# Optimization experiments

Measured on AMD Instinct MI355X. Metric: run time of the kernel, lower is better.

## Reference

```python
import jax, jax.numpy as jnp
import numpy as np

B, F, H, OUT, S = 32768, 256, 128, 64, 6
RELAX, EPS, BN_EPS = 1.5, 1e-05, 1e-05
SQRT_HALF = 0.7071067811865476


def _bn(h, g, b):
    # training-mode BatchNorm1d: biased batch statistics over dim 0
    m = h.mean(axis=0)
    v = h.var(axis=0)
    return (h - m) * jax.lax.rsqrt(v + BN_EPS) * g + b


def _tfrm(x, W, g, b, glu_act=True):
    h = _bn(x @ W, g, b)
    if glu_act:
        d = h.shape[1] // 2
        h = h[:, :d] * jax.nn.sigmoid(h[:, d:])
    return h


def setup_inputs() -> dict:
    key = jax.random.key(0)
    ks = jax.random.split(key, 6)
    f32 = jnp.float32
    return {
        "x": jax.random.normal(ks[0], (B, F), f32),
        "enc_g": jnp.ones((F,), f32), "enc_b": jnp.zeros((F,), f32),
        "W1": jax.random.normal(ks[1], (F, 2 * H), f32) * 0.05,
        "g1": jnp.ones((2 * H,), f32), "b1": jnp.zeros((2 * H,), f32),
        "W2": jax.random.normal(ks[2], (H, 2 * H), f32) * 0.05,
        "g2": jnp.ones((2 * H,), f32), "b2": jnp.zeros((2 * H,), f32),
        "W3": jax.random.normal(ks[3], (S, H, 2 * H), f32) * 0.05,
        "g3": jnp.ones((S, 2 * H), f32), "b3": jnp.zeros((S, 2 * H), f32),
        "W4": jax.random.normal(ks[4], (S, H, 2 * H), f32) * 0.05,
        "g4": jnp.ones((S, 2 * H), f32), "b4": jnp.zeros((S, 2 * H), f32),
        "Wc": jax.random.normal(ks[5], (S - 1, OUT, F), f32) * 0.05,
        "gc": jnp.ones((S - 1, F), f32), "bc": jnp.zeros((S - 1, F), f32),
    }


def reference(x, enc_g, enc_b, W1, g1, b1, W2, g2, b2, W3, g3, b3,
              W4, g4, b4, Wc, gc, bc):
    x = _bn(x, enc_g, enc_b)                      # [B, F]
    masked = x
    compl = jnp.ones((x.shape[0], F), x.dtype)    # complementary aggregated mask
    agg_out, agg_entropy = [], []
    for ni in range(S):
        h = _tfrm(masked, W1, g1, b1)                             # [B, H]
        h = (_tfrm(h, W2, g2, b2) + h) * SQRT_HALF
        h = (_tfrm(h, W3[ni], g3[ni], b3[ni]) + h) * SQRT_HALF
        h = (_tfrm(h, W4[ni], g4[ni], b4[ni]) + h) * SQRT_HALF
        if ni > 0:
            # NOTE: source uses x (not h) here -- replicated faithfully
            agg_out.append(jax.nn.relu(x[:, :OUT]))
        fc = h[:, OUT:]                                           # [B, OUT]
        if ni < S - 1:
            coef = _tfrm(fc, Wc[ni], gc[ni], bc[ni], glu_act=False)  # [B, F]
            mask_values = jax.nn.softmax(coef * compl, axis=1)
            compl = compl * (RELAX - mask_values)
            agg_entropy.append(
                jnp.mean(jnp.sum(-mask_values * jnp.log(mask_values + EPS), axis=1))
                / (S - 1))
            masked = mask_values * x
    out = jnp.sum(jnp.stack(agg_out, axis=0), axis=0)   # [B, OUT]
    entropy = jnp.sum(jnp.stack(agg_entropy))           # scalar
    return (out, entropy)
```

## Files before the change

kernel.cpp:

```cpp
#include <hip/hip_runtime.h>
#include <math.h>

#define BSZ   32768
#define FDIM  256
#define HDIM  128
#define OUTD  64
#define SQRT_HALF 0.70710678118654752f
#define BN_EPS 1e-5f
#define SM_EPS 1e-5f
#define INV_B (1.0f / 32768.0f)
#define NCPY  8
#define SLOT  (NCPY * 512)

typedef __attribute__((ext_vector_type(8))) short bf16x8;
typedef __attribute__((ext_vector_type(4))) short bf16x4;
typedef __attribute__((ext_vector_type(4))) float f32x4;

__device__ __forceinline__ float b2f(unsigned short u) {
    return __uint_as_float(((unsigned int)u) << 16);
}
__device__ __forceinline__ unsigned short f2b(float f) {
    unsigned int u = __float_as_uint(f);
    u += 0x7fff + ((u >> 16) & 1);
    return (unsigned short)(u >> 16);
}

__device__ __forceinline__ void async16(const void* g, void* l) {
    __builtin_amdgcn_global_load_lds(
        (const __attribute__((address_space(1))) void*)(uintptr_t)g,
        (__attribute__((address_space(3))) void*)(unsigned int)(uintptr_t)l,
        16, 0, 0);
}

__device__ inline float waveMaxAll(float v) {
#pragma unroll
    for (int m = 32; m > 0; m >>= 1) v = fmaxf(v, __shfl_xor(v, m, 64));
    return v;
}
__device__ inline float waveSumAll(float v) {
#pragma unroll
    for (int m = 32; m > 0; m >>= 1) v += __shfl_xor(v, m, 64);
    return v;
}

__global__ __launch_bounds__(256) void prep_w(
    const float* __restrict__ W1, const float* __restrict__ W2,
    const float* __restrict__ W3, const float* __restrict__ W4,
    const float* __restrict__ Wc,
    unsigned short* __restrict__ W1t, unsigned short* __restrict__ W2t,
    unsigned short* __restrict__ W3t, unsigned short* __restrict__ W4t,
    unsigned short* __restrict__ Wct)
{
    const int m = blockIdx.x, kz = blockIdx.y, n = threadIdx.x;
    const float* src; unsigned short* dst; int K;
    if (m == 0)      { src = W1;                        dst = W1t;               K = 256; }
    else if (m == 1) { src = W2;                        dst = W2t;               K = 128; }
    else if (m < 7)  { int i = m - 2;  src = W3 + (size_t)i * 128 * 256; dst = W3t + (size_t)i * 32768; K = 128; }
    else if (m < 12) { int i = m - 7;  src = W4 + (size_t)i * 128 * 256; dst = W4t + (size_t)i * 32768; K = 128; }
    else             { int i = m - 12; src = Wc + (size_t)i * 64 * 256;  dst = Wct + (size_t)i * 16384; K = 64; }
    const int k0 = kz * 32;
    if (k0 >= K) return;
    for (int k = k0; k < k0 + 32; ++k)
        dst[(size_t)n * K + k] = f2b(src[(size_t)k * 256 + n]);
}

__global__ __launch_bounds__(256) void colstats(const float* __restrict__ X,
                                                float* __restrict__ st0) {
    __shared__ float red[4][512];
    const int sub = threadIdx.x >> 6;
    const int c4  = (threadIdx.x & 63) << 2;
    float s[4] = {0.f, 0.f, 0.f, 0.f}, q[4] = {0.f, 0.f, 0.f, 0.f};
#pragma unroll 8
    for (int i = 0; i < 8; ++i) {
        const int row = blockIdx.x * 32 + i * 4 + sub;
        float4 v = *(const float4*)(X + (size_t)row * 256 + c4);
        s[0] += v.x; q[0] += v.x * v.x;
        s[1] += v.y; q[1] += v.y * v.y;
        s[2] += v.z; q[2] += v.z * v.z;
        s[3] += v.w; q[3] += v.w * v.w;
    }
#pragma unroll
    for (int e = 0; e < 4; ++e) {
        red[sub][c4 + e] = s[e];
        red[sub][256 + c4 + e] = q[e];
    }
    __syncthreads();
    const int t = threadIdx.x;
    const int cp = (blockIdx.x & (NCPY - 1)) * 512;
    float sS = red[0][t] + red[1][t] + red[2][t] + red[3][t];
    float sQ = red[0][256 + t] + red[1][256 + t] + red[2][256 + t] + red[3][256 + t];
    atomicAdd(&st0[cp + t], sS);
    atomicAdd(&st0[cp + 256 + t], sQ);
}

__global__ __launch_bounds__(256) void norm_x(const float* __restrict__ x,
                                              const float* __restrict__ st0,
                                              const float* __restrict__ g,
                                              const float* __restrict__ b,
                                              unsigned short* __restrict__ xb,
                                              float* __restrict__ out) {
    const int i4 = blockIdx.x * 256 + threadIdx.x;
    const int row = i4 >> 6, c4 = (i4 & 63) << 2;
    float4 xv = *(const float4*)(x + (size_t)row * 256 + c4);
    float sS[4] = {0.f, 0.f, 0.f, 0.f}, sQ[4] = {0.f, 0.f, 0.f, 0.f};
#pragma unroll
    for (int cp = 0; cp < NCPY; ++cp) {
        float4 a = *(const float4*)&st0[cp * 512 + c4];
        float4 q = *(const float4*)&st0[cp * 512 + 256 + c4];
        sS[0] += a.x; sS[1] += a.y; sS[2] += a.z; sS[3] += a.w;
        sQ[0] += q.x; sQ[1] += q.y; sQ[2] += q.z; sQ[3] += q.w;
    }
    float4 gv = *(const float4*)&g[c4];
    float4 bv = *(const float4*)&b[c4];
    const float* xp = (const float*)&xv;
    const float* gp = (const float*)&gv; const float* bp = (const float*)&bv;
    float n[4];
    ushort4 ob;
    unsigned short* obp = (unsigned short*)&ob;
#pragma unroll
    for (int e = 0; e < 4; ++e) {
        float mean = sS[e] * INV_B;
        float var  = sQ[e] * INV_B - mean * mean;
        float sc   = gp[e] * rsqrtf(var + BN_EPS);
        float sh   = bp[e] - mean * sc;
        n[e] = xp[e] * sc + sh;
        obp[e] = f2b(n[e]);
    }
    *(ushort4*)(xb + (size_t)row * 256 + c4) = ob;
    if (c4 < OUTD) {
        float4 ov = make_float4(5.0f * fmaxf(n[0], 0.f), 5.0f * fmaxf(n[1], 0.f),
                                5.0f * fmaxf(n[2], 0.f), 5.0f * fmaxf(n[3], 0.f));
        *(float4*)(out + (size_t)row * OUTD + c4) = ov;
    }
}

__device__ __forceinline__ void gemm_epilogue(
    f32x4 (&acc)[2][4], int row0, int wave, int lane, int tid, int bcp,
    float* redS, float* redQ,
    unsigned short* __restrict__ Pout, float* __restrict__ statsOut)
{
    const int fm = lane & 15;
    const int orow = row0 + (lane >> 4) * 4;
    const int ocol = wave * 64 + fm;
#pragma unroll
    for (int i = 0; i < 2; ++i)
#pragma unroll
        for (int j = 0; j < 4; ++j)
#pragma unroll
            for (int r = 0; r < 4; ++r)
                Pout[(size_t)(orow + i * 16 + r) * 256 + (ocol + j * 16)] = f2b(acc[i][j][r]);

#pragma unroll
    for (int j = 0; j < 4; ++j) {
        float s = 0.f, q = 0.f;
#pragma unroll
        for (int i = 0; i < 2; ++i)
#pragma unroll
            for (int r = 0; r < 4; ++r) {
                float v = acc[i][j][r];
                s += v; q += v * v;
            }
        s += __shfl_xor(s, 16, 64); s += __shfl_xor(s, 32, 64);
        q += __shfl_xor(q, 16, 64); q += __shfl_xor(q, 32, 64);
        if (lane < 16) {
            redS[wave * 64 + j * 16 + lane] = s;
            redQ[wave * 64 + j * 16 + lane] = q;
        }
    }
    __syncthreads();
    atomicAdd(&statsOut[bcp + tid], redS[tid]);
    atomicAdd(&statsOut[bcp + 256 + tid], redQ[tid]);
}

__global__ __launch_bounds__(256) void gemm_bf16(
    const unsigned short* __restrict__ A,
    const unsigned short* __restrict__ Wt, int K,
    unsigned short* __restrict__ P,
    float* __restrict__ statsOut)
{
    __shared__ short As[32 * 32];
    __shared__ short Bs[256 * 32];
    __shared__ float redS[256], redQ[256];

    const int tid  = threadIdx.x;
    const int wave = tid >> 6;
    const int lane = tid & 63;
    const int row0 = blockIdx.x * 32;
    const int bcp  = (blockIdx.x & (NCPY - 1)) * 512;

    const int sr = lane >> 2;
    const int sc = (lane & 3) * 8;
    const int fm = lane & 15;
    const int fq = (lane >> 4) * 8;

    f32x4 acc[2][4];
#pragma unroll
    for (int i = 0; i < 2; ++i)
#pragma unroll
        for (int j = 0; j < 4; ++j)
            acc[i][j] = (f32x4){0.f, 0.f, 0.f, 0.f};

    for (int k0 = 0; k0 < K; k0 += 32) {
        if (wave < 2)
            async16(A + (size_t)(row0 + wave * 16 + sr) * K + k0 + sc,
                    (void*)(As + wave * 512 + lane * 8));
#pragma unroll
        for (int t = 0; t < 4; ++t) {
            const int wr = wave * 64 + t * 16 + sr;
            async16(Wt + (size_t)wr * K + k0 + sc,
                    (void*)(Bs + (wave * 4 + t) * 512 + lane * 8));
        }
        __syncthreads();

        bf16x8 af[2], bfr[4];
#pragma unroll
        for (int i = 0; i < 2; ++i)
            af[i] = *(const bf16x8*)(As + (i * 16 + fm) * 32 + fq);
#pragma unroll
        for (int j = 0; j < 4; ++j)
            bfr[j] = *(const bf16x8*)(Bs + (wave * 64 + j * 16 + fm) * 32 + fq);
#pragma unroll
        for (int i = 0; i < 2; ++i)
#pragma unroll
            for (int j = 0; j < 4; ++j)
                acc[i][j] = __builtin_amdgcn_mfma_f32_16x16x32_bf16(af[i], bfr[j], acc[i][j], 0, 0, 0);
        __syncthreads();
    }

    gemm_epilogue(acc, row0, wave, lane, tid, bcp, redS, redQ, P, statsOut);
}

template <int MODE>
__global__ __launch_bounds__(256) void gemm_mask(
    const unsigned short* Pc,
    const float* __restrict__ cstats,
    const float* __restrict__ gc, const float* __restrict__ bc,
    const unsigned short* __restrict__ xb,
    unsigned short* __restrict__ cmpl,
    float* __restrict__ ent,
    const unsigned short* __restrict__ Wt,
    unsigned short* Pout,
    float* __restrict__ statsOut)
{
    __shared__ short Am[32 * 256];
    __shared__ short Bs[256 * 32];
    __shared__ float redS[256], redQ[256];
    __shared__ float tScl[256], tShf[256];
    __shared__ float went[4];

    const int tid  = threadIdx.x;
    const int wave = tid >> 6;
    const int lane = tid & 63;
    const int row0 = blockIdx.x * 32;
    const int bcp  = (blockIdx.x & (NCPY - 1)) * 512;

    const int sr = lane >> 2;
    const int sc = (lane & 3) * 8;

#pragma unroll
    for (int t = 0; t < 4; ++t) {
        const int wr = wave * 64 + t * 16 + sr;
        async16(Wt + (size_t)wr * 256 + sc,
                (void*)(Bs + (wave * 4 + t) * 512 + lane * 8));
    }

    {
        float s = 0.f, q = 0.f;
#pragma unroll
        for (int cp = 0; cp < NCPY; ++cp) {
            s += cstats[cp * 512 + tid];
            q += cstats[cp * 512 + 256 + tid];
        }
        float mean = s * INV_B, var = q * INV_B - mean * mean;
        float scl_ = gc[tid] * rsqrtf(var + BN_EPS);
        tScl[tid] = scl_;
        tShf[tid] = bc[tid] - mean * scl_;
    }
    __syncthreads();

    const int r  = tid >> 3;
    const int cq = tid & 7;
    const size_t grow = (size_t)(row0 + r) * 256;

    float l[32];
    float mx = -1e30f;
#pragma unroll
    for (int e = 0; e < 4; ++e) {
        const int c = cq * 32 + e * 8;
        bf16x8 pv = *(const bf16x8*)(Pc + grow + c);
        bf16x8 cv;
        if (MODE) cv = *(const bf16x8*)(cmpl + grow + c);
        float4 s0 = *(const float4*)&tScl[c], s1 = *(const float4*)&tScl[c + 4];
        float4 h0 = *(const float4*)&tShf[c], h1 = *(const float4*)&tShf[c + 4];
        const float* sp0 = (const float*)&s0; const float* sp1 = (const float*)&s1;
        const float* hp0 = (const float*)&h0; const float* hp1 = (const float*)&h1;
#pragma unroll
        for (int t = 0; t < 8; ++t) {
            float scl_ = (t < 4) ? sp0[t] : sp1[t - 4];
            float shf_ = (t < 4) ? hp0[t] : hp1[t - 4];
            float cl = MODE ? b2f((unsigned short)cv[t]) : 1.0f;
            float v = (b2f((unsigned short)pv[t]) * scl_ + shf_) * cl;
            l[e * 8 + t] = v;
            mx = fmaxf(mx, v);
        }
    }
    mx = fmaxf(mx, __shfl_xor(mx, 1, 64));
    mx = fmaxf(mx, __shfl_xor(mx, 2, 64));
    mx = fmaxf(mx, __shfl_xor(mx, 4, 64));

    float ssum = 0.f;
#pragma unroll
    for (int i = 0; i < 32; ++i) { l[i] = __expf(l[i] - mx); ssum += l[i]; }
    ssum += __shfl_xor(ssum, 1, 64);
    ssum += __shfl_xor(ssum, 2, 64);
    ssum += __shfl_xor(ssum, 4, 64);
    const float inv = 1.0f / ssum;

    float et = 0.f;
#pragma unroll
    for (int e = 0; e < 4; ++e) {
        const int c = cq * 32 + e * 8;
        bf16x8 xv = *(const bf16x8*)(xb + grow + c);
        bf16x8 cv2;
        if (MODE) cv2 = *(const bf16x8*)(cmpl + grow + c);
        bf16x8 mo, co;
#pragma unroll
        for (int t = 0; t < 8; ++t) {
            float m = l[e * 8 + t] * inv;
            et -= m * __logf(m + SM_EPS);
            float cl = MODE ? b2f((unsigned short)cv2[t]) : 1.0f;
            co[t] = (short)f2b(cl * (1.5f - m));
            mo[t] = (short)f2b(m * b2f((unsigned short)xv[t]));
        }
        *(bf16x8*)(cmpl + grow + c) = co;
        unsigned int byte = (unsigned int)(r * 512 + c * 2);
        byte ^= ((unsigned int)(r & 7)) << 4;
        *(bf16x8*)((char*)Am + byte) = mo;
    }
    et += __shfl_xor(et, 1, 64);
    et += __shfl_xor(et, 2, 64);
    et += __shfl_xor(et, 4, 64);
    float wet = waveSumAll(et) * 0.125f;
    if (lane == 0) went[wave] = wet;
    __syncthreads();
    if (tid == 0) {
        float v = went[0] + went[1] + went[2] + went[3];
        atomicAdd(&ent[(blockIdx.x & 255) << 5], v * (INV_B * 0.2f));
    }

    const int fm = lane & 15;
    const int fq = (lane >> 4) * 8;

    f32x4 acc[2][4];
#pragma unroll
    for (int i = 0; i < 2; ++i)
#pragma unroll
        for (int j = 0; j < 4; ++j)
            acc[i][j] = (f32x4){0.f, 0.f, 0.f, 0.f};

    for (int k0 = 0; k0 < 256; k0 += 32) {
        bf16x8 af[2], bfr[4];
#pragma unroll
        for (int i = 0; i < 2; ++i) {
            const int row = i * 16 + fm;
            unsigned int byte = (unsigned int)(row * 512 + (k0 + fq) * 2);
            byte ^= ((unsigned int)(row & 7)) << 4;
            af[i] = *(const bf16x8*)((const char*)Am + byte);
        }
#pragma unroll
        for (int j = 0; j < 4; ++j)
            bfr[j] = *(const bf16x8*)(Bs + (wave * 64 + j * 16 + fm) * 32 + fq);
#pragma unroll
        for (int i = 0; i < 2; ++i)
#pragma unroll
            for (int j = 0; j < 4; ++j)
                acc[i][j] = __builtin_amdgcn_mfma_f32_16x16x32_bf16(af[i], bfr[j], acc[i][j], 0, 0, 0);
        __syncthreads();
        if (k0 + 32 < 256) {
#pragma unroll
            for (int t = 0; t < 4; ++t) {
                const int wr = wave * 64 + t * 16 + sr;
                async16(Wt + (size_t)wr * 256 + (k0 + 32) + sc,
                        (void*)(Bs + (wave * 4 + t) * 512 + lane * 8));
            }
            __syncthreads();
        }
    }

    gemm_epilogue(acc, row0, wave, lane, tid, bcp, redS, redQ, Pout, statsOut);
}

template <bool RES, bool WRITE_H>
__global__ __launch_bounds__(256) void gemm_glu(
    const unsigned short* __restrict__ Pprev,
    const float* __restrict__ pstats,
    const float* __restrict__ pg,
    const float* __restrict__ pb,
    const unsigned short* __restrict__ res,
    int colOff,
    const unsigned short* __restrict__ Wt, int K,
    unsigned short* __restrict__ Pout,
    float* __restrict__ statsOut,
    unsigned short* __restrict__ hOut)
{
    __shared__ short As[32 * 32];
    __shared__ short Bs[256 * 32];
    __shared__ float redS[256], redQ[256];
    __shared__ float tScA[128], tShA[128], tScG[128], tShG[128];

    const int tid  = threadIdx.x;
    const int wave = tid >> 6;
    const int lane = tid & 63;
    const int row0 = blockIdx.x * 32;
    const int bcp  = (blockIdx.x & (NCPY - 1)) * 512;

    if (tid < K) {
        const int ch = colOff + tid;
        const int cg = ch + 128;
        float sA = 0.f, qA = 0.f, sG = 0.f, qG = 0.f;
#pragma unroll
        for (int cp = 0; cp < NCPY; ++cp) {
            const float* p = pstats + cp * 512;
            sA += p[ch]; qA += p[256 + ch];
            sG += p[cg]; qG += p[256 + cg];
        }
        float ma = sA * INV_B, va = qA * INV_B - ma * ma;
        float scA = pg[ch] * rsqrtf(va + BN_EPS);
        tScA[tid] = scA; tShA[tid] = pb[ch] - ma * scA;
        float mg = sG * INV_B, vg = qG * INV_B - mg * mg;
        float scG = pg[cg] * rsqrtf(vg + BN_EPS);
        tScG[tid] = scG; tShG[tid] = pb[cg] - mg * scG;
    }
    __syncthreads();

    const int sr = lane >> 2;
    const int sc = (lane & 3) * 8;
    const int ar = tid >> 3;
    const int ac = (tid & 7) * 4;
    const int fm = lane & 15;
    const int fq = (lane >> 4) * 8;

    f32x4 acc[2][4];
#pragma unroll
    for (int i = 0; i < 2; ++i)
#pragma unroll
        for (int j = 0; j < 4; ++j)
            acc[i][j] = (f32x4){0.f, 0.f, 0.f, 0.f};

    for (int k0 = 0; k0 < K; k0 += 32) {
#pragma unroll
        for (int t = 0; t < 4; ++t) {
            const int wr = wave * 64 + t * 16 + sr;
            async16(Wt + (size_t)wr * K + k0 + sc,
                    (void*)(Bs + (wave * 4 + t) * 512 + lane * 8));
        }

        {
            const int kk = k0 + ac;
            const size_t grow = (size_t)(row0 + ar);

            bf16x4 lo = *(const bf16x4*)(Pprev + grow * 256 + colOff + kk);
            bf16x4 hi = *(const bf16x4*)(Pprev + grow * 256 + colOff + kk + 128);
            bf16x4 rv;
            if (RES) rv = *(const bf16x4*)(res + grow * 128 + kk);

            float4 a0 = *(const float4*)&tScA[kk];
            float4 h0 = *(const float4*)&tShA[kk];
            float4 g0 = *(const float4*)&tScG[kk];
            float4 s0 = *(const float4*)&tShG[kk];
            float scA[4] = {a0.x, a0.y, a0.z, a0.w};
            float shA[4] = {h0.x, h0.y, h0.z, h0.w};
            float scG[4] = {g0.x, g0.y, g0.z, g0.w};
            float shG[4] = {s0.x, s0.y, s0.z, s0.w};

            bf16x4 o4;
#pragma unroll
            for (int e = 0; e < 4; ++e) {
                float na = b2f((unsigned short)lo[e]) * scA[e] + shA[e];
                float ng = b2f((unsigned short)hi[e]) * scG[e] + shG[e];
                float v = na * (1.0f / (1.0f + __expf(-ng)));
                if (RES) v = (v + b2f((unsigned short)rv[e])) * SQRT_HALF;
                o4[e] = (short)f2b(v);
            }
            *(bf16x4*)(As + ar * 32 + ac) = o4;
            if (WRITE_H)
                *(bf16x4*)(hOut + grow * 128 + kk) = o4;
        }
        __syncthreads();

        bf16x8 af[2], bfr[4];
#pragma unroll
        for (int i = 0; i < 2; ++i)
            af[i] = *(const bf16x8*)(As + (i * 16 + fm) * 32 + fq);
#pragma unroll
        for (int j = 0; j < 4; ++j)
            bfr[j] = *(const bf16x8*)(Bs + (wave * 64 + j * 16 + fm) * 32 + fq);
#pragma unroll
        for (int i = 0; i < 2; ++i)
#pragma unroll
            for (int j = 0; j < 4; ++j)
                acc[i][j] = __builtin_amdgcn_mfma_f32_16x16x32_bf16(af[i], bfr[j], acc[i][j], 0, 0, 0);
        __syncthreads();
    }

    gemm_epilogue(acc, row0, wave, lane, tid, bcp, redS, redQ, Pout, statsOut);
}

__global__ __launch_bounds__(256) void coef_ent(const unsigned short* __restrict__ Pc,
                                                const float* __restrict__ stats,
                                                const float* __restrict__ gc,
                                                const float* __restrict__ bc,
                                                const unsigned short* __restrict__ cmpl,
                                                float* __restrict__ ent) {
    const int w    = threadIdx.x >> 6;
    const int lane = threadIdx.x & 63;
    const int row  = blockIdx.x * 4 + w;
    const int c    = lane << 2;
    __shared__ float went[4];

    float sS[4] = {0.f, 0.f, 0.f, 0.f}, sQ[4] = {0.f, 0.f, 0.f, 0.f};
#pragma unroll
    for (int cp = 0; cp < NCPY; ++cp) {
        float4 a = *(const float4*)&stats[cp * 512 + c];
        float4 q = *(const float4*)&stats[cp * 512 + 256 + c];
        sS[0] += a.x; sS[1] += a.y; sS[2] += a.z; sS[3] += a.w;
        sQ[0] += q.x; sQ[1] += q.y; sQ[2] += q.z; sQ[3] += q.w;
    }
    float4 gv = *(const float4*)&gc[c];
    float4 bv = *(const float4*)&bc[c];
    const float* gvv = (const float*)&gv; const float* bvv = (const float*)&bv;

    float scl[4], shf[4];
#pragma unroll
    for (int e = 0; e < 4; ++e) {
        float mean = sS[e] * INV_B, var = sQ[e] * INV_B - mean * mean;
        scl[e] = gvv[e] * rsqrtf(var + BN_EPS);
        shf[e] = bvv[e] - mean * scl[e];
    }

    const size_t idx = (size_t)row * 256 + c;
    ushort4 pu = *(const ushort4*)(Pc + idx);
    const unsigned short* puv = (const unsigned short*)&pu;
    ushort4 cu = *(const ushort4*)(cmpl + idx);
    const unsigned short* cuv = (const unsigned short*)&cu;

    float l[4];
#pragma unroll
    for (int e = 0; e < 4; ++e)
        l[e] = (b2f(puv[e]) * scl[e] + shf[e]) * b2f(cuv[e]);

    float mx = waveMaxAll(fmaxf(fmaxf(l[0], l[1]), fmaxf(l[2], l[3])));
    float e0 = __expf(l[0] - mx), e1 = __expf(l[1] - mx),
          e2 = __expf(l[2] - mx), e3 = __expf(l[3] - mx);
    float inv = 1.0f / waveSumAll(e0 + e1 + e2 + e3);

    float m[4] = {e0 * inv, e1 * inv, e2 * inv, e3 * inv};

    float et = -m[0] * __logf(m[0] + SM_EPS) - m[1] * __logf(m[1] + SM_EPS)
             - m[2] * __logf(m[2] + SM_EPS) - m[3] * __logf(m[3] + SM_EPS);
    et = waveSumAll(et);
    if (lane == 0) went[w] = et;
    __syncthreads();
    if (threadIdx.x == 0) {
        float v = went[0] + went[1] + went[2] + went[3];
        atomicAdd(&ent[(blockIdx.x & 255) << 5], v * (INV_B * 0.2f));
    }
}

__global__ __launch_bounds__(64) void write_ent(const float* __restrict__ ent,
                                                float* __restrict__ dst) {
    const int lane = threadIdx.x;
    float v = 0.f;
#pragma unroll
    for (int i = 0; i < 4; ++i) v += ent[(lane + 64 * i) << 5];
    v = waveSumAll(v);
    if (lane == 0) dst[0] = v;
}

extern "C" void kernel_launch(void* const* d_in, const int* in_sizes, int n_in,
                              void* d_out, int out_size, void* d_ws, size_t ws_size,
                              hipStream_t stream) {
    const float* x     = (const float*)d_in[0];
    const float* enc_g = (const float*)d_in[1];
    const float* enc_b = (const float*)d_in[2];
    const float* W1 = (const float*)d_in[3];
    const float* g1 = (const float*)d_in[4];
    const float* b1 = (const float*)d_in[5];
    const float* W2 = (const float*)d_in[6];
    const float* g2 = (const float*)d_in[7];
    const float* b2 = (const float*)d_in[8];
    const float* W3 = (const float*)d_in[9];
    const float* g3 = (const float*)d_in[10];
    const float* b3 = (const float*)d_in[11];
    const float* W4 = (const float*)d_in[12];
    const float* g4 = (const float*)d_in[13];
    const float* b4 = (const float*)d_in[14];
    const float* Wc = (const float*)d_in[15];
    const float* gc = (const float*)d_in[16];
    const float* bc = (const float*)d_in[17];
    float* out = (float*)d_out;

    const size_t NBF = (size_t)BSZ * FDIM;
    const size_t NBH = (size_t)BSZ * HDIM;

    unsigned short* xb     = (unsigned short*)d_ws;
    unsigned short* masked = xb + NBF;
    unsigned short* Pb1    = masked + NBF;
    unsigned short* h1     = Pb1 + NBF;
    unsigned short* h2     = h1 + NBH;
    unsigned short* h3     = h2 + NBH;
    unsigned short* cmpl   = h3 + NBH;
    unsigned short* W1t    = cmpl + NBF;
    unsigned short* W2t    = W1t + 65536;
    unsigned short* W3t    = W2t + 32768;
    unsigned short* W4t    = W3t + 163840;
    unsigned short* Wct    = W4t + 163840;
    float* stats = (float*)(Wct + 81920);
    float* ent   = stats + 26 * SLOT;

    unsigned short* Pb2 = masked;

    hipMemsetAsync(stats, 0, (26 * SLOT + 256 * 32) * sizeof(float), stream);

    prep_w<<<dim3(17, 8), 256, 0, stream>>>(W1, W2, W3, W4, Wc, W1t, W2t, W3t, W4t, Wct);
    colstats<<<1024, 256, 0, stream>>>(x, stats);
    norm_x<<<8192, 256, 0, stream>>>(x, stats, enc_g, enc_b, xb, out);

    for (int ni = 0; ni < 5; ++ni) {
        float* s1 = stats + (size_t)(1 + ni * 5 + 0) * SLOT;
        float* s2 = stats + (size_t)(1 + ni * 5 + 1) * SLOT;
        float* s3 = stats + (size_t)(1 + ni * 5 + 2) * SLOT;
        float* s4 = stats + (size_t)(1 + ni * 5 + 3) * SLOT;
        float* s5 = stats + (size_t)(1 + ni * 5 + 4) * SLOT;

        if (ni == 0) {
            gemm_bf16<<<1024, 256, 0, stream>>>(xb, W1t, 256, Pb1, s1);
        } else {
            float* s5p = stats + (size_t)(1 + (ni - 1) * 5 + 4) * SLOT;
            if (ni == 1)
                gemm_mask<0><<<1024, 256, 0, stream>>>(
                    Pb1, s5p, gc, bc, xb, cmpl, ent, W1t, Pb1, s1);
            else
                gemm_mask<1><<<1024, 256, 0, stream>>>(
                    Pb1, s5p, gc + (ni - 1) * 256, bc + (ni - 1) * 256,
                    xb, cmpl, ent, W1t, Pb1, s1);
        }

        gemm_glu<false, true><<<1024, 256, 0, stream>>>(
            Pb1, s1, g1, b1, nullptr, 0, W2t, 128, Pb2, s2, h1);
        gemm_glu<true, true><<<1024, 256, 0, stream>>>(
            Pb2, s2, g2, b2, h1, 0, W3t + (size_t)ni * 32768, 128, Pb1, s3, h2);
        gemm_glu<true, true><<<1024, 256, 0, stream>>>(
            Pb1, s3, g3 + ni * 256, b3 + ni * 256, h2, 0,
            W4t + (size_t)ni * 32768, 128, Pb2, s4, h3);
        gemm_glu<true, false><<<1024, 256, 0, stream>>>(
            Pb2, s4, g4 + ni * 256, b4 + ni * 256, h3 + 64, 64,
            Wct + (size_t)ni * 16384, 64, Pb1, s5, nullptr);
    }

    coef_ent<<<BSZ / 4, 256, 0, stream>>>(
        Pb1, stats + (size_t)(1 + 4 * 5 + 4) * SLOT,
        gc + 4 * 256, bc + 4 * 256, cmpl, ent);

    write_ent<<<1, 64, 0, stream>>>(ent, out + (size_t)BSZ * OUTD);
}
```

Measured before the change: 565.3 us.

## Fuse whole pipeline into one persistent kernel with software grid barriers

Replaces the sequence of per-stage kernel launches with a single persistent kernel of 1024 blocks. Each block owns 32 rows and keeps its activations in LDS across stages, and a software grid barrier synchronises the batch-norm statistics between GEMM stages. This removes launch overhead and the global round trips for intermediate activations. In exchange it depends on all blocks being co-resident, which is checked through an occupancy query with a fallback to the old path. The spin barrier has a timeout, and the 25-plus grid syncs add their own latency.

```diff
diff --git a/kernel.cpp b/kernel.cpp
--- a/kernel.cpp
+++ b/kernel.cpp
@@ -11,6 +11,9 @@
 #define INV_B (1.0f / 32768.0f)
 #define NCPY  8
 #define SLOT  (NCPY * 512)
+#define GRID  1024
+
+#define SWZ(r, cb) ((((r) << 9) + (cb)) ^ (((r) & 7) << 4))
 
 typedef __attribute__((ext_vector_type(8))) short bf16x8;
 typedef __attribute__((ext_vector_type(4))) short bf16x4;
@@ -41,6 +44,454 @@
 #pragma unroll
     for (int m = 32; m > 0; m >>= 1) v += __shfl_xor(v, m, 64);
     return v;
+}
+
+__device__ __forceinline__ void grid_sync_sw(unsigned int* bar, unsigned int nb) {
+    __syncthreads();
+    if (threadIdx.x == 0) {
+        __threadfence();
+        unsigned int gen = __hip_atomic_load(bar + 1, __ATOMIC_RELAXED, __HIP_MEMORY_SCOPE_AGENT);
+        unsigned int arr = __hip_atomic_fetch_add(bar, 1u, __ATOMIC_ACQ_REL, __HIP_MEMORY_SCOPE_AGENT);
+        if (arr == nb - 1) {
+            __hip_atomic_store(bar, 0u, __ATOMIC_RELAXED, __HIP_MEMORY_SCOPE_AGENT);
+            __hip_atomic_fetch_add(bar + 1, 1u, __ATOMIC_RELEASE, __HIP_MEMORY_SCOPE_AGENT);
+        } else {
+            long spin = 0;
+            while (__hip_atomic_load(bar + 1, __ATOMIC_ACQUIRE, __HIP_MEMORY_SCOPE_AGENT) == gen) {
+                if (++spin > (1L << 24)) break;
+                __builtin_amdgcn_s_sleep(2);
+            }
+        }
+        __threadfence();
+    }
+    __syncthreads();
+}
+
+__device__ __forceinline__ void stage_B(short* Bs, const unsigned short* __restrict__ Wt,
+                                        int K, int k0, int wave, int lane) {
+    const int sr = lane >> 2;
+    const int sc = (lane & 3) * 8;
+#pragma unroll
+    for (int t = 0; t < 4; ++t) {
+        const int wr = wave * 64 + t * 16 + sr;
+        async16(Wt + (size_t)wr * K + k0 + sc, (void*)(Bs + (wave * 4 + t) * 512 + lane * 8));
+    }
+}
+
+__device__ __forceinline__ void gemm_core(const short* buf, short* Bs,
+                                          const unsigned short* __restrict__ Wt, int K,
+                                          int wave, int lane, f32x4 (&acc)[2][4]) {
+    const int fm = lane & 15;
+    const int fq = (lane >> 4) * 8;
+#pragma unroll
+    for (int i = 0; i < 2; ++i)
+#pragma unroll
+        for (int j = 0; j < 4; ++j)
+            acc[i][j] = (f32x4){0.f, 0.f, 0.f, 0.f};
+
+    for (int k0 = 0; k0 < K; k0 += 32) {
+        __syncthreads();
+        bf16x8 af[2], bfr[4];
+#pragma unroll
+        for (int i = 0; i < 2; ++i)
+            af[i] = *(const bf16x8*)((const char*)buf + SWZ(i * 16 + fm, (k0 + fq) * 2));
+#pragma unroll
+        for (int j = 0; j < 4; ++j)
+            bfr[j] = *(const bf16x8*)(Bs + (wave * 64 + j * 16 + fm) * 32 + fq);
+#pragma unroll
+        for (int i = 0; i < 2; ++i)
+#pragma unroll
+            for (int j = 0; j < 4; ++j)
+                acc[i][j] = __builtin_amdgcn_mfma_f32_16x16x32_bf16(af[i], bfr[j], acc[i][j], 0, 0, 0);
+        __syncthreads();
+        if (k0 + 32 < K) stage_B(Bs, Wt, K, k0 + 32, wave, lane);
+    }
+}
+
+__device__ __forceinline__ void stage_epilogue(f32x4 (&acc)[2][4], short* buf,
+                                               float* redS, float* redQ,
+                                               float* __restrict__ statsOut,
+                                               int wave, int lane, int tid, int bcp) {
+    const int fm = lane & 15;
+    const int row4 = (lane >> 4) * 4;
+    const int ocol = wave * 64 + fm;
+#pragma unroll
+    for (int i = 0; i < 2; ++i)
+#pragma unroll
+        for (int j = 0; j < 4; ++j)
+#pragma unroll
+            for (int r = 0; r < 4; ++r)
+                *(short*)((char*)buf + SWZ(row4 + i * 16 + r, (ocol + j * 16) * 2)) =
+                    (short)f2b(acc[i][j][r]);
+
+#pragma unroll
+    for (int j = 0; j < 4; ++j) {
+        float s = 0.f, q = 0.f;
+#pragma unroll
+        for (int i = 0; i < 2; ++i)
+#pragma unroll
+            for (int r = 0; r < 4; ++r) {
+                float v = acc[i][j][r];
+                s += v; q += v * v;
+            }
+        s += __shfl_xor(s, 16, 64); s += __shfl_xor(s, 32, 64);
+        q += __shfl_xor(q, 16, 64); q += __shfl_xor(q, 32, 64);
+        if (lane < 16) {
+            redS[wave * 64 + j * 16 + lane] = s;
+            redQ[wave * 64 + j * 16 + lane] = q;
+        }
+    }
+    __syncthreads();
+    atomicAdd(&statsOut[bcp + tid], redS[tid]);
+    atomicAdd(&statsOut[bcp + 256 + tid], redQ[tid]);
+}
+
+__device__ __forceinline__ void build_tbl_glu(const float* __restrict__ st,
+                                              const float* __restrict__ pg,
+                                              const float* __restrict__ pb,
+                                              int colOff, int K, int tid, float* tbl) {
+    if (tid < K) {
+        const int ch = colOff + tid;
+        const int cg = ch + 128;
+        float sA = 0.f, qA = 0.f, sG = 0.f, qG = 0.f;
+#pragma unroll
+        for (int cp = 0; cp < NCPY; ++cp) {
+            const float* p = st + cp * 512;
+            sA += p[ch]; qA += p[256 + ch];
+            sG += p[cg]; qG += p[256 + cg];
+        }
+        float ma = sA * INV_B, va = qA * INV_B - ma * ma;
+        float scA = pg[ch] * rsqrtf(va + BN_EPS);
+        tbl[tid] = scA; tbl[K + tid] = pb[ch] - ma * scA;
+        float mg = sG * INV_B, vg = qG * INV_B - mg * mg;
+        float scG = pg[cg] * rsqrtf(vg + BN_EPS);
+        tbl[2 * K + tid] = scG; tbl[3 * K + tid] = pb[cg] - mg * scG;
+    }
+    __syncthreads();
+}
+
+__device__ __forceinline__ void build_tbl_mask(const float* __restrict__ st,
+                                               const float* __restrict__ gcp,
+                                               const float* __restrict__ bcp_,
+                                               int tid, float* tbl) {
+    float s = 0.f, q = 0.f;
+#pragma unroll
+    for (int cp = 0; cp < NCPY; ++cp) {
+        s += st[cp * 512 + tid];
+        q += st[cp * 512 + 256 + tid];
+    }
+    float mean = s * INV_B, var = q * INV_B - mean * mean;
+    float scl = gcp[tid] * rsqrtf(var + BN_EPS);
+    tbl[tid] = scl;
+    tbl[256 + tid] = bcp_[tid] - mean * scl;
+    __syncthreads();
+}
+
+template <int K, bool RES, bool WH, int RB>
+__device__ __forceinline__ void glu_prologue(short* buf, const float* tbl,
+                                             int tid, int colOff, bf16x4* h) {
+    const int ar = tid >> 3;
+    const int ac = (tid & 7) * 4;
+#pragma unroll
+    for (int c = 0; c < K / 32; ++c) {
+        const int kk = c * 32 + ac;
+        bf16x4 lo = *(const bf16x4*)((const char*)buf + SWZ(ar, (colOff + kk) * 2));
+        bf16x4 hi = *(const bf16x4*)((const char*)buf + SWZ(ar, (colOff + kk + 128) * 2));
+        float4 a0 = *(const float4*)&tbl[kk];
+        float4 h0 = *(const float4*)&tbl[K + kk];
+        float4 g0 = *(const float4*)&tbl[2 * K + kk];
+        float4 s0 = *(const float4*)&tbl[3 * K + kk];
+        const float scA[4] = {a0.x, a0.y, a0.z, a0.w};
+        const float shA[4] = {h0.x, h0.y, h0.z, h0.w};
+        const float scG[4] = {g0.x, g0.y, g0.z, g0.w};
+        const float shG[4] = {s0.x, s0.y, s0.z, s0.w};
+        bf16x4 o4;
+#pragma unroll
+        for (int e = 0; e < 4; ++e) {
+            float na = b2f((unsigned short)lo[e]) * scA[e] + shA[e];
+            float ng = b2f((unsigned short)hi[e]) * scG[e] + shG[e];
+            float v = na * (1.0f / (1.0f + __expf(-ng)));
+            if (RES) v = (v + b2f((unsigned short)h[RB + c][e])) * SQRT_HALF;
+            o4[e] = (short)f2b(v);
+        }
+        *(bf16x4*)((char*)buf + SWZ(ar, kk * 2)) = o4;
+        if (WH) h[c] = o4;
+    }
+}
+
+template <int MODE>
+__device__ __forceinline__ void mask_phase(short* buf, const float* tbl,
+                                           const unsigned short* __restrict__ xb,
+                                           unsigned short* cmpl, float* ent, float* went,
+                                           int tid, int wave, int lane, int row0, int bid) {
+    const int r = tid >> 3;
+    const int cq = tid & 7;
+    const size_t grow = (size_t)(row0 + r) * 256;
+
+    float l[32];
+    float mx = -1e30f;
+#pragma unroll
+    for (int e = 0; e < 4; ++e) {
+        const int c = cq * 32 + e * 8;
+        bf16x8 pv = *(const bf16x8*)((const char*)buf + SWZ(r, c * 2));
+        bf16x8 cv;
+        if (MODE != 0) cv = *(const bf16x8*)(cmpl + grow + c);
+        float4 s0 = *(const float4*)&tbl[c], s1 = *(const float4*)&tbl[c + 4];
+        float4 h0 = *(const float4*)&tbl[256 + c], h1 = *(const float4*)&tbl[256 + c + 4];
+        const float* sp0 = (const float*)&s0; const float* sp1 = (const float*)&s1;
+        const float* hp0 = (const float*)&h0; const float* hp1 = (const float*)&h1;
+#pragma unroll
+        for (int t = 0; t < 8; ++t) {
+            float scl = (t < 4) ? sp0[t] : sp1[t - 4];
+            float shf = (t < 4) ? hp0[t] : hp1[t - 4];
+            float cl = (MODE != 0) ? b2f((unsigned short)cv[t]) : 1.0f;
+            float v = (b2f((unsigned short)pv[t]) * scl + shf) * cl;
+            l[e * 8 + t] = v;
+            mx = fmaxf(mx, v);
+        }
+    }
+    mx = fmaxf(mx, __shfl_xor(mx, 1, 64));
+    mx = fmaxf(mx, __shfl_xor(mx, 2, 64));
+    mx = fmaxf(mx, __shfl_xor(mx, 4, 64));
+
+    float ssum = 0.f;
+#pragma unroll
+    for (int i = 0; i < 32; ++i) { l[i] = __expf(l[i] - mx); ssum += l[i]; }
+    ssum += __shfl_xor(ssum, 1, 64);
+    ssum += __shfl_xor(ssum, 2, 64);
+    ssum += __shfl_xor(ssum, 4, 64);
+    const float inv = 1.0f / ssum;
+
+    float et = 0.f;
+#pragma unroll
+    for (int e = 0; e < 4; ++e) {
+        const int c = cq * 32 + e * 8;
+        bf16x8 xv, cv2;
+        if (MODE != 2) xv = *(const bf16x8*)(xb + grow + c);
+        if (MODE == 1) cv2 = *(const bf16x8*)(cmpl + grow + c);
+        bf16x8 mo, co;
+#pragma unroll
+        for (int t = 0; t < 8; ++t) {
+            float m = l[e * 8 + t] * inv;
+            et -= m * __logf(m + SM_EPS);
+            if (MODE != 2) {
+                float cl = (MODE == 1) ? b2f((unsigned short)cv2[t]) : 1.0f;
+                co[t] = (short)f2b(cl * (1.5f - m));
+                mo[t] = (short)f2b(m * b2f((unsigned short)xv[t]));
+            }
+        }
+        if (MODE != 2) {
+            *(bf16x8*)(cmpl + grow + c) = co;
+            *(bf16x8*)((char*)buf + SWZ(r, c * 2)) = mo;
+        }
+    }
+    et += __shfl_xor(et, 1, 64);
+    et += __shfl_xor(et, 2, 64);
+    et += __shfl_xor(et, 4, 64);
+    float wet = waveSumAll(et) * 0.125f;
+    if (lane == 0) went[wave] = wet;
+    __syncthreads();
+    if (tid == 0) {
+        float v = went[0] + went[1] + went[2] + went[3];
+        atomicAdd(&ent[(bid & 255) << 5], v * (INV_B * 0.2f));
+    }
+}
+
+__global__ __launch_bounds__(256, 4) void mega(
+    const float* __restrict__ x,
+    const float* __restrict__ enc_g, const float* __restrict__ enc_b,
+    const float* __restrict__ g1, const float* __restrict__ b1,
+    const float* __restrict__ g2, const float* __restrict__ b2,
+    const float* __restrict__ g3, const float* __restrict__ b3,
+    const float* __restrict__ g4, const float* __restrict__ b4,
+    const float* __restrict__ gc, const float* __restrict__ bc,
+    const float* __restrict__ W1f, const float* __restrict__ W2f,
+    const float* __restrict__ W3f, const float* __restrict__ W4f,
+    const float* __restrict__ Wcf,
+    unsigned short* __restrict__ W1t, unsigned short* __restrict__ W2t,
+    unsigned short* __restrict__ W3t, unsigned short* __restrict__ W4t,
+    unsigned short* __restrict__ Wct,
+    unsigned short* __restrict__ xb, unsigned short* __restrict__ cmpl,
+    float* __restrict__ stats, float* __restrict__ ent,
+    unsigned int* __restrict__ bar,
+    float* __restrict__ out)
+{
+#define GSYNC() grid_sync_sw(bar, GRID)
+
+    __shared__ short buf[32 * 256];
+    __shared__ short Bs[256 * 32];
+    __shared__ float redS[256], redQ[256];
+    __shared__ float tbl[512];
+    __shared__ float went[4];
+
+    const int tid  = threadIdx.x;
+    const int wave = tid >> 6;
+    const int lane = tid & 63;
+    const int bid  = blockIdx.x;
+    const int row0 = bid * 32;
+    const int bcp  = (bid & (NCPY - 1)) * 512;
+
+    if (bid < 136) {
+        const int m = bid >> 3, kz = bid & 7, n = tid;
+        const float* src; unsigned short* dst; int K;
+        if (m == 0)      { src = W1f;                        dst = W1t;               K = 256; }
+        else if (m == 1) { src = W2f;                        dst = W2t;               K = 128; }
+        else if (m < 7)  { int i = m - 2;  src = W3f + (size_t)i * 128 * 256; dst = W3t + (size_t)i * 32768; K = 128; }
+        else if (m < 12) { int i = m - 7;  src = W4f + (size_t)i * 128 * 256; dst = W4t + (size_t)i * 32768; K = 128; }
+        else             { int i = m - 12; src = Wcf + (size_t)i * 64 * 256;  dst = Wct + (size_t)i * 16384; K = 64; }
+        const int k0 = kz * 32;
+        if (k0 < K)
+            for (int k = k0; k < k0 + 32; ++k)
+                dst[(size_t)n * K + k] = f2b(src[(size_t)k * 256 + n]);
+    }
+    {
+        float* red = (float*)buf;
+        const int sub = wave;
+        const int c4  = lane << 2;
+        float s[4] = {0.f, 0.f, 0.f, 0.f}, q[4] = {0.f, 0.f, 0.f, 0.f};
+#pragma unroll 8
+        for (int i = 0; i < 8; ++i) {
+            const int row = row0 + i * 4 + sub;
+            float4 v = *(const float4*)(x + (size_t)row * 256 + c4);
+            s[0] += v.x; q[0] += v.x * v.x;
+            s[1] += v.y; q[1] += v.y * v.y;
+            s[2] += v.z; q[2] += v.z * v.z;
+            s[3] += v.w; q[3] += v.w * v.w;
+        }
+#pragma unroll
+        for (int e = 0; e < 4; ++e) {
+            red[sub * 512 + c4 + e] = s[e];
+            red[sub * 512 + 256 + c4 + e] = q[e];
+        }
+        __syncthreads();
+        float sS = red[tid] + red[512 + tid] + red[1024 + tid] + red[1536 + tid];
+        float sQ = red[256 + tid] + red[768 + tid] + red[1280 + tid] + red[1792 + tid];
+        atomicAdd(&stats[bcp + tid], sS);
+        atomicAdd(&stats[bcp + 256 + tid], sQ);
+    }
+    GSYNC();
+
+    stage_B(Bs, W1t, 256, 0, wave, lane);
+    {
+        float s = 0.f, q = 0.f;
+#pragma unroll
+        for (int cp = 0; cp < NCPY; ++cp) {
+            s += stats[cp * 512 + tid];
+            q += stats[cp * 512 + 256 + tid];
+        }
+        float mean = s * INV_B, var = q * INV_B - mean * mean;
+        float scl = enc_g[tid] * rsqrtf(var + BN_EPS);
+        tbl[tid] = scl;
+        tbl[256 + tid] = enc_b[tid] - mean * scl;
+    }
+    __syncthreads();
+    {
+        const int r = tid >> 3, cq = tid & 7;
+        const size_t grow = (size_t)(row0 + r) * 256;
+#pragma unroll
+        for (int e = 0; e < 4; ++e) {
+            const int c = cq * 32 + e * 8;
+            float4 xa = *(const float4*)(x + grow + c);
+            float4 xc = *(const float4*)(x + grow + c + 4);
+            const float xv[8] = {xa.x, xa.y, xa.z, xa.w, xc.x, xc.y, xc.z, xc.w};
+            float4 s0 = *(const float4*)&tbl[c], s1 = *(const float4*)&tbl[c + 4];
+            float4 f0 = *(const float4*)&tbl[256 + c], f1 = *(const float4*)&tbl[256 + c + 4];
+            const float sc[8] = {s0.x, s0.y, s0.z, s0.w, s1.x, s1.y, s1.z, s1.w};
+            const float sh[8] = {f0.x, f0.y, f0.z, f0.w, f1.x, f1.y, f1.z, f1.w};
+            float n[8];
+            bf16x8 o8;
+#pragma unroll
+            for (int t = 0; t < 8; ++t) {
+                n[t] = xv[t] * sc[t] + sh[t];
+                o8[t] = (short)f2b(n[t]);
+            }
+            *(bf16x8*)((char*)buf + SWZ(r, c * 2)) = o8;
+            *(bf16x8*)(xb + grow + c) = o8;
+            if (c < OUTD) {
+                float4 o1 = make_float4(5.f * fmaxf(n[0], 0.f), 5.f * fmaxf(n[1], 0.f),
+                                        5.f * fmaxf(n[2], 0.f), 5.f * fmaxf(n[3], 0.f));
+                float4 o2 = make_float4(5.f * fmaxf(n[4], 0.f), 5.f * fmaxf(n[5], 0.f),
+                                        5.f * fmaxf(n[6], 0.f), 5.f * fmaxf(n[7], 0.f));
+                *(float4*)(out + (size_t)(row0 + r) * OUTD + c) = o1;
+                *(float4*)(out + (size_t)(row0 + r) * OUTD + c + 4) = o2;
+            }
+        }
+    }
+
+    f32x4 acc[2][4];
+    bf16x4 h[4];
+
+    for (int ni = 0; ni < 5; ++ni) {
+        float* s1 = stats + (size_t)(1 + ni * 5 + 0) * SLOT;
+        float* s2 = stats + (size_t)(1 + ni * 5 + 1) * SLOT;
+        float* s3 = stats + (size_t)(1 + ni * 5 + 2) * SLOT;
+        float* s4 = stats + (size_t)(1 + ni * 5 + 3) * SLOT;
+        float* s5 = stats + (size_t)(1 + ni * 5 + 4) * SLOT;
+
+        if (ni > 0) {
+            stage_B(Bs, W1t, 256, 0, wave, lane);
+            float* s5p = stats + (size_t)(1 + (ni - 1) * 5 + 4) * SLOT;
+            build_tbl_mask(s5p, gc + (ni - 1) * 256, bc + (ni - 1) * 256, tid, tbl);
+            if (ni == 1)
+                mask_phase<0>(buf, tbl, xb, cmpl, ent, went, tid, wave, lane, row0, bid);
+            else
+                mask_phase<1>(buf, tbl, xb, cmpl, ent, went, tid, wave, lane, row0, bid);
+        }
+        gemm_core(buf, Bs, W1t, 256, wave, lane, acc);
+        stage_epilogue(acc, buf, redS, redQ, s1, wave, lane, tid, bcp);
+        GSYNC();
+
+        stage_B(Bs, W2t, 128, 0, wave, lane);
+        build_tbl_glu(s1, g1, b1, 0, 128, tid, tbl);
+        glu_prologue<128, false, true, 0>(buf, tbl, tid, 0, h);
+        gemm_core(buf, Bs, W2t, 128, wave, lane, acc);
+        stage_epilogue(acc, buf, redS, redQ, s2, wave, lane, tid, bcp);
+        GSYNC();
+
+        {
+            const unsigned short* Wt = W3t + (size_t)ni * 32768;
+            stage_B(Bs, Wt, 128, 0, wave, lane);
+            build_tbl_glu(s2, g2, b2, 0, 128, tid, tbl);
+            glu_prologue<128, true, true, 0>(buf, tbl, tid, 0, h);
+            gemm_core(buf, Bs, Wt, 128, wave, lane, acc);
+            stage_epilogue(acc, buf, redS, redQ, s3, wave, lane, tid, bcp);
+        }
+        GSYNC();
+
+        {
+            const unsigned short* Wt = W4t + (size_t)ni * 32768;
+            stage_B(Bs, Wt, 128, 0, wave, lane);
+            build_tbl_glu(s3, g3 + ni * 256, b3 + ni * 256, 0, 128, tid, tbl);
+            glu_prologue<128, true, true, 0>(buf, tbl, tid, 0, h);
+            gemm_core(buf, Bs, Wt, 128, wave, lane, acc);
+            stage_epilogue(acc, buf, redS, redQ, s4, wave, lane, tid, bcp);
+        }
+        GSYNC();
+
+        {
+            const unsigned short* Wt = Wct + (size_t)ni * 16384;
+            stage_B(Bs, Wt, 64, 0, wave, lane);
+            build_tbl_glu(s4, g4 + ni * 256, b4 + ni * 256, 64, 64, tid, tbl);
+            glu_prologue<64, true, false, 2>(buf, tbl, tid, 64, h);
+            gemm_core(buf, Bs, Wt, 64, wave, lane, acc);
+            stage_epilogue(acc, buf, redS, redQ, s5, wave, lane, tid, bcp);
+        }
+        GSYNC();
+    }
+
+    build_tbl_mask(stats + (size_t)(1 + 4 * 5 + 4) * SLOT,
+                   gc + 4 * 256, bc + 4 * 256, tid, tbl);
+    mask_phase<2>(buf, tbl, xb, cmpl, ent, went, tid, wave, lane, row0, bid);
+    GSYNC();
+
+    if (bid == 0 && wave == 0) {
+        float v = 0.f;
+#pragma unroll
+        for (int i = 0; i < 4; ++i) v += ent[(lane + 64 * i) << 5];
+        v = waveSumAll(v);
+        if (lane == 0) out[(size_t)BSZ * OUTD] = v;
+    }
+#undef GSYNC
 }
 
 __global__ __launch_bounds__(256) void prep_w(
@@ -617,10 +1068,31 @@
     unsigned short* Wct    = W4t + 163840;
     float* stats = (float*)(Wct + 81920);
     float* ent   = stats + 26 * SLOT;
+    unsigned int* bar = (unsigned int*)masked;
 
     unsigned short* Pb2 = masked;
 
+    static int s_ok = -1;
+    if (s_ok < 0) {
+        int occ = 0, mpc = 0, dev = 0;
+        hipGetDevice(&dev);
+        hipDeviceProp_t prop;
+        if (hipGetDeviceProperties(&prop, dev) == hipSuccess) mpc = prop.multiProcessorCount;
+        if (hipOccupancyMaxActiveBlocksPerMultiprocessor(
+                &occ, reinterpret_cast<const void*>(mega), 256, 0) != hipSuccess) occ = 0;
+        s_ok = (occ >= 4 && occ * mpc >= GRID) ? 1 : 0;
+    }
+
     hipMemsetAsync(stats, 0, (26 * SLOT + 256 * 32) * sizeof(float), stream);
+
+    if (s_ok) {
+        hipMemsetAsync(bar, 0, 2 * sizeof(unsigned int), stream);
+        mega<<<GRID, 256, 0, stream>>>(
+            x, enc_g, enc_b, g1, b1, g2, b2, g3, b3, g4, b4, gc, bc,
+            W1, W2, W3, W4, Wc, W1t, W2t, W3t, W4t, Wct,
+            xb, cmpl, stats, ent, bar, out);
+        return;
+    }
 
     prep_w<<<dim3(17, 8), 256, 0, stream>>>(W1, W2, W3, W4, Wc, W1t, W2t, W3t, W4t, Wct);
     colstats<<<1024, 256, 0, stream>>>(x, stats);
```

Measured after the change: 565.5 us. Within noise of the previous version (+0.0%).
